# Kernel tuning notes

Hardware: AMD Instinct MI355X
Metric: run time of the kernel (lower is better)

Reference implementation:

```python
import jax, jax.numpy as jnp
import numpy as np

# dims (must match input_specs / init_kwargs)
B, N, L, D = 4, 2000, 32, 64
H, ND, K, DOUT = 4, 64, 20, 64  # num_heads, node_dim, topk, out_dim
EPS = 1e-8


def setup_inputs() -> dict:
    key = jax.random.key(0)
    ks = jax.random.split(key, 10)
    lim_emb = float(np.sqrt(6.0 / (N + ND)))  # xavier_uniform-ish for embeddings
    lim_l1 = float(np.sqrt(1.0 / H))          # torch Linear default-ish
    lim_l2 = float(np.sqrt(1.0 / (2 * H)))
    lim_w = float(np.sqrt(6.0 / (D + DOUT)))
    return {
        "x": jax.random.normal(ks[0], (B, N, L, D), dtype=jnp.float32),
        "e1": jax.random.uniform(ks[1], (H, N, ND), minval=-lim_emb, maxval=lim_emb, dtype=jnp.float32),
        "e2": jax.random.uniform(ks[2], (H, ND, N), minval=-lim_emb, maxval=lim_emb, dtype=jnp.float32),
        "temperature": jnp.ones((H,), dtype=jnp.float32),
        "ew1": jax.random.uniform(ks[3], (H, 2 * H), minval=-lim_l1, maxval=lim_l1, dtype=jnp.float32),
        "eb1": jax.random.uniform(ks[4], (2 * H,), minval=-lim_l1, maxval=lim_l1, dtype=jnp.float32),
        "ew2": jax.random.uniform(ks[5], (2 * H, 1), minval=-lim_l2, maxval=lim_l2, dtype=jnp.float32),
        "eb2": jax.random.uniform(ks[6], (1,), minval=-lim_l2, maxval=lim_l2, dtype=jnp.float32),
        "weight": jax.random.uniform(ks[7], (D, DOUT), minval=-lim_w, maxval=lim_w, dtype=jnp.float32),
        "bias": jnp.zeros((DOUT,), dtype=jnp.float32),
    }


def _graph_learner(e1, e2, temperature, ew1, eb1, ew2, eb2):
    # per-head scores: (H, N, N)
    scores = jnp.einsum("hnd,hdm->hnm", e1, e2)
    adj = jax.nn.softmax(jax.nn.relu(scores) / temperature[:, None, None], axis=-1)
    # topk sparsification along each row (dim=1 in torch == last axis here)
    _, idx = jax.lax.top_k(adj, K)  # (H, N, K)
    mask = jnp.zeros_like(adj).at[
        jnp.arange(H)[:, None, None], jnp.arange(N)[None, :, None], idx
    ].set(1.0)
    adj = adj * mask
    adj = adj / (jnp.sum(adj, axis=-1, keepdims=True) + EPS)
    # edge encoder MLP over head dim (dropout is identity in eval mode)
    feats = jnp.transpose(adj, (1, 2, 0))              # (N, N, H)
    hid = jax.nn.relu(feats @ ew1 + eb1)               # (N, N, 2H)
    ew = (hid @ ew2 + eb2)[..., 0]                     # (N, N)
    final_adj = jax.nn.sigmoid(ew) * jnp.mean(adj, axis=0)
    return final_adj, adj


def reference(x, e1, e2, temperature, ew1, eb1, ew2, eb2, weight, bias):
    final_adj, _ = _graph_learner(e1, e2, temperature, ew1, eb1, ew2, eb2)
    Bv, Nv, Lv, Dv = x.shape
    xr = jnp.transpose(x, (0, 2, 1, 3)).reshape(Bv * Lv, Nv, Dv)  # (B*L, N, D)
    support = xr @ weight                                          # (B*L, N, Dout)
    # adj.t() @ support  ->  out[b,i,:] = sum_j adj[j,i] * support[b,j,:]
    out = jnp.einsum("ji,bjd->bid", final_adj, support) + bias
    out = jnp.transpose(out.reshape(Bv, Lv, Nv, -1), (0, 2, 1, 3))  # (B, N, L, Dout)
    return out, final_adj
```

## Files before the change

kernel.cpp:

```cpp
#include <hip/hip_runtime.h>

#define NB   2000
#define HH   4
#define KK   20
#define KP   2048
#define GA   4
#define EPSF 1e-8f

typedef unsigned short ushort;
typedef unsigned long long ull;
using short8   = __attribute__((ext_vector_type(8))) short;
using floatx4  = __attribute__((ext_vector_type(4))) float;
using ushortx4 = __attribute__((ext_vector_type(4))) unsigned short;
using ushortx8 = __attribute__((ext_vector_type(8))) unsigned short;

__device__ inline ushort f2bf(float f) {
    unsigned u = __builtin_bit_cast(unsigned, f);
    u += 0x7fffu + ((u >> 16) & 1u);
    return (ushort)(u >> 16);
}

__device__ __forceinline__ void gload_lds16(const ushort* g, ushort* l) {
    __builtin_amdgcn_global_load_lds(
        (const __attribute__((address_space(1))) void*)g,
        (__attribute__((address_space(3))) void*)l, 16, 0, 0);
}

template<int CTRL>
__device__ __forceinline__ float dppmax(float x) {
    int xi = __builtin_bit_cast(int, x);
    int yi = __builtin_amdgcn_update_dpp(xi, xi, CTRL, 0xF, 0xF, false);
    return fmaxf(x, __builtin_bit_cast(float, yi));
}

__device__ __forceinline__ float wavemax63(float x) {
    x = dppmax<0x111>(x);
    x = dppmax<0x112>(x);
    x = dppmax<0x114>(x);
    x = dppmax<0x118>(x);
    x = dppmax<0x142>(x);
    x = dppmax<0x143>(x);
    return x;
}

#define COMP(v,i) ((i)==0?(v).x:(i)==1?(v).y:(i)==2?(v).z:(v).w)

__global__ __launch_bounds__(512, 4) void k_scores_topk(
    const float* __restrict__ e1, const float* __restrict__ e2,
    const float* __restrict__ temperature,
    int* __restrict__ topk_idx, float* __restrict__ topk_val)
{
    const int h  = blockIdx.y;
    const int n0 = blockIdx.x * GA;
    const int t  = threadIdx.x;
    const int w  = t >> 6, lane = t & 63;

    __shared__ float e1s[GA][64];
    __shared__ float scoresS[GA][2048];
    __shared__ float red[GA][4];
    __shared__ ull   lists[4][GA][KK + 1];
    __shared__ float selpv[GA][KK];
    __shared__ int   seli[GA][KK];
    __shared__ float ssum[GA];

    if (t < 256)
        e1s[t >> 6][t & 63] = e1[(size_t)(h * NB + n0 + (t >> 6)) * 64 + (t & 63)];
    __syncthreads();

    const float rtemp = 1.f / temperature[h];
    const float* __restrict__ e2h = e2 + (size_t)h * 64 * NB;

    {
        const int mb1 = w * 256 + lane * 4;
        const int ml1 = (mb1 < NB) ? mb1 : (NB - 4);

        float acc[GA][4];
#pragma unroll
        for (int r = 0; r < GA; r++)
#pragma unroll
            for (int c = 0; c < 4; c++) acc[r][c] = 0.f;

        for (int d4 = 0; d4 < 64; d4 += 4) {
            float4 ev0 = *(const float4*)&e1s[0][d4];
            float4 ev1 = *(const float4*)&e1s[1][d4];
            float4 ev2 = *(const float4*)&e1s[2][d4];
            float4 ev3 = *(const float4*)&e1s[3][d4];
#pragma unroll
            for (int dd = 0; dd < 4; dd++) {
                float4 a = *(const float4*)(e2h + (size_t)(d4 + dd) * NB + ml1);
                float f0 = COMP(ev0, dd), f1 = COMP(ev1, dd);
                float f2 = COMP(ev2, dd), f3 = COMP(ev3, dd);
                acc[0][0] += f0*a.x; acc[0][1] += f0*a.y; acc[0][2] += f0*a.z; acc[0][3] += f0*a.w;
                acc[1][0] += f1*a.x; acc[1][1] += f1*a.y; acc[1][2] += f1*a.z; acc[1][3] += f1*a.w;
                acc[2][0] += f2*a.x; acc[2][1] += f2*a.y; acc[2][2] += f2*a.z; acc[2][3] += f2*a.w;
                acc[3][0] += f3*a.x; acc[3][1] += f3*a.y; acc[3][2] += f3*a.z; acc[3][3] += f3*a.w;
            }
        }

#pragma unroll
        for (int r = 0; r < GA; r++) {
            float4 v; v.x = acc[r][0]; v.y = acc[r][1]; v.z = acc[r][2]; v.w = acc[r][3];
            *(float4*)&scoresS[r][mb1] = v;
        }
    }
    __syncthreads();

    if (w < 4) {
        const int  mbase = w * 512 + lane * 8;
        const bool valid = (mbase < NB);

        float acc[GA][8];
#pragma unroll
        for (int r = 0; r < GA; r++) {
            float4 lo = *(const float4*)&scoresS[r][mbase];
            float4 hi = *(const float4*)&scoresS[r][mbase + 4];
            acc[r][0] = lo.x; acc[r][1] = lo.y; acc[r][2] = lo.z; acc[r][3] = lo.w;
            acc[r][4] = hi.x; acc[r][5] = hi.y; acc[r][6] = hi.z; acc[r][7] = hi.w;
        }

#pragma unroll
        for (int r = 0; r < GA; r++) {
            float tvm = -1.f;
#pragma unroll
            for (int k = 0; k < 8; k++) {
                float v = valid ? fmaxf(acc[r][k], 0.f) * rtemp : -1.f;
                acc[r][k] = v;
                tvm = fmaxf(tvm, v);
            }
            tvm = wavemax63(tvm);
            if (lane == 63) red[r][w] = tvm;
        }

        float lm[GA]; int ak[GA];
#pragma unroll
        for (int r = 0; r < GA; r++) {
            float l = acc[r][0]; int a = 0;
#pragma unroll
            for (int k = 1; k < 8; k++)
                if (acc[r][k] > l) { l = acc[r][k]; a = k; }
            lm[r] = l; ak[r] = a;
        }

        for (int round = 0; round < KK; round++) {
            float M[GA];
#pragma unroll
            for (int r = 0; r < GA; r++) M[r] = lm[r];
#pragma unroll
            for (int r = 0; r < GA; r++) M[r] = dppmax<0x111>(M[r]);
#pragma unroll
            for (int r = 0; r < GA; r++) M[r] = dppmax<0x112>(M[r]);
#pragma unroll
            for (int r = 0; r < GA; r++) M[r] = dppmax<0x114>(M[r]);
#pragma unroll
            for (int r = 0; r < GA; r++) M[r] = dppmax<0x118>(M[r]);
#pragma unroll
            for (int r = 0; r < GA; r++) M[r] = dppmax<0x142>(M[r]);
#pragma unroll
            for (int r = 0; r < GA; r++) M[r] = dppmax<0x143>(M[r]);
#pragma unroll
            for (int r = 0; r < GA; r++)
                M[r] = __builtin_bit_cast(float,
                         __builtin_amdgcn_readlane(__builtin_bit_cast(int, M[r]), 63));
#pragma unroll
            for (int r = 0; r < GA; r++) {
                ull ball = __ballot(lm[r] == M[r]);
                int wl   = __ffsll(ball) - 1;
                if (lane == wl) {
                    int gidx = mbase + ak[r];
                    lists[w][r][round] =
                        ((ull)__float_as_uint(M[r]) << 32) | (unsigned)~gidx;
#pragma unroll
                    for (int k = 0; k < 8; k++) if (k == ak[r]) acc[r][k] = -2.f;
                    float l = acc[r][0]; int a = 0;
#pragma unroll
                    for (int k = 1; k < 8; k++)
                        if (acc[r][k] > l) { l = acc[r][k]; a = k; }
                    lm[r] = l; ak[r] = a;
                }
            }
        }
#pragma unroll
        for (int r = 0; r < GA; r++)
            if (lane == 0) lists[w][r][KK] = 0ULL;
    }
    __syncthreads();

    if (t < GA) {
        const int r = t;
        float mx = fmaxf(fmaxf(red[r][0], red[r][1]), fmaxf(red[r][2], red[r][3]));
        int p0 = 0, p1 = 0, p2 = 0, p3 = 0;
        ull h0 = lists[0][r][0], h1 = lists[1][r][0];
        ull h2 = lists[2][r][0], h3 = lists[3][r][0];
        float ss = 0.f;
        for (int q = 0; q < KK; q++) {
            ull a_ = h0 >= h1 ? h0 : h1; int wa = h0 >= h1 ? 0 : 1;
            ull b_ = h2 >= h3 ? h2 : h3; int wb = h2 >= h3 ? 2 : 3;
            ull bk = a_ >= b_ ? a_ : b_; int bw = a_ >= b_ ? wa : wb;
            float tvv = __uint_as_float((unsigned)(bk >> 32));
            float pv  = __expf(tvv - mx);
            selpv[r][q] = pv;
            seli[r][q]  = (int)~(unsigned)bk;
            ss += pv;
            if      (bw == 0) h0 = lists[0][r][++p0];
            else if (bw == 1) h1 = lists[1][r][++p1];
            else if (bw == 2) h2 = lists[2][r][++p2];
            else              h3 = lists[3][r][++p3];
        }
        ssum[r] = ss;
    }
    __syncthreads();

    if (t < GA * KK) {
        int r = t / KK, q = t % KK;
        int o = (h * NB + n0 + r) * KK + q;
        topk_idx[o] = seli[r][q];
        topk_val[o] = selpv[r][q] / (ssum[r] + EPSF);
    }
}

__global__ __launch_bounds__(256) void k_final_adj(
    const int* __restrict__ topk_idx, const float* __restrict__ topk_val,
    const float* __restrict__ ew1, const float* __restrict__ eb1,
    const float* __restrict__ ew2, const float* __restrict__ eb2,
    float* __restrict__ fadj_out, ushort* __restrict__ faT_b)
{
    const int i = blockIdx.x;
    const int t = threadIdx.x;

    __shared__ float rows[HH][NB];
    __shared__ float w1[32];
    __shared__ float b1[8];
    __shared__ float w2[8];
    __shared__ float b2v;

    for (int k = t; k < HH * NB; k += 256) ((float*)rows)[k] = 0.f;
    if (t < 32) w1[t] = ew1[t];
    if (t < 8)  { b1[t] = eb1[t]; w2[t] = ew2[t]; }
    if (t == 0) b2v = eb2[0];
    __syncthreads();

    if (t < HH * KK) {
        int h = t / KK, r = t % KK;
        int o = (h * NB + i) * KK + r;
        rows[h][topk_idx[o]] = topk_val[o];
    }
    __syncthreads();

#pragma unroll
    for (int k = 0; k < 8; k++) {
        int j = k * 256 + t;
        if (j < NB) {
            float f0 = rows[0][j], f1 = rows[1][j], f2 = rows[2][j], f3 = rows[3][j];
            float mean = (f0 + f1 + f2 + f3) * 0.25f;
            float outv = 0.f;
            if (mean > 0.f) {
                float ewv = b2v;
#pragma unroll
                for (int c = 0; c < 8; c++) {
                    float hid = f0 * w1[c] + f1 * w1[8 + c] + f2 * w1[16 + c] + f3 * w1[24 + c] + b1[c];
                    hid = fmaxf(hid, 0.f);
                    ewv += hid * w2[c];
                }
                float sig = 1.f / (1.f + expf(-ewv));
                outv = sig * mean;
                faT_b[(size_t)j * KP + i] = f2bf(outv);
            }
            fadj_out[(size_t)i * NB + j] = outv;
        }
    }
}

__global__ __launch_bounds__(256) void k_support_t(
    const float* __restrict__ x, const float* __restrict__ w,
    ushort* __restrict__ ST)
{
    const int jt = blockIdx.x;
    const int bl = blockIdx.y;
    const int b_ = bl >> 5, l = bl & 31;
    const int t  = threadIdx.x;

    __shared__ float  xs[64][65];
    __shared__ float  ws[64 * 64];
    __shared__ ushort ob[64 * 65];

    for (int k = t; k < 4096; k += 256) ws[k] = w[k];

    {
        const float* xb = x + (size_t)b_ * 4096000 + (size_t)l * 64;
#pragma unroll
        for (int p = 0; p < 4; p++) {
            int q  = p * 256 + t;
            int jl = q >> 4, f4 = q & 15;
            int jg = jt * 64 + jl;
            int jc = jg < NB ? jg : (NB - 1);
            *(float4*)&xs[jl][f4 * 4] =
                *(const float4*)(xb + (size_t)jc * 2048 + f4 * 4);
        }
    }
    __syncthreads();

    const int dq = t & 15;
    const int g  = t >> 4;
    float acc[4][4];
#pragma unroll
    for (int r = 0; r < 4; r++)
#pragma unroll
        for (int c = 0; c < 4; c++) acc[r][c] = 0.f;

    for (int dd = 0; dd < 64; dd++) {
        float4 w4 = *(const float4*)&ws[dd * 64 + dq * 4];
#pragma unroll
        for (int r = 0; r < 4; r++) {
            float xv = xs[g * 4 + r][dd];
            acc[r][0] += xv * w4.x;
            acc[r][1] += xv * w4.y;
            acc[r][2] += xv * w4.z;
            acc[r][3] += xv * w4.w;
        }
    }

#pragma unroll
    for (int r = 0; r < 4; r++) {
        int jl = g * 4 + r;
        bool jvalid = (jt * 64 + jl) < NB;
        ushort* dst = &ob[jl * 65 + dq * 4];
        dst[0] = jvalid ? f2bf(acc[r][0]) : (ushort)0;
        dst[1] = jvalid ? f2bf(acc[r][1]) : (ushort)0;
        dst[2] = jvalid ? f2bf(acc[r][2]) : (ushort)0;
        dst[3] = jvalid ? f2bf(acc[r][3]) : (ushort)0;
    }
    __syncthreads();

#pragma unroll
    for (int p = 0; p < 2; p++) {
        int q = p * 256 + t;
        int rc = q >> 3, s = q & 7;
        ushortx8 o;
#pragma unroll
        for (int k = 0; k < 8; k++) o[k] = ob[(s * 8 + k) * 65 + rc];
        *(ushortx8*)&ST[(size_t)(bl * 64 + rc) * KP + jt * 64 + s * 8] = o;
    }
}

__global__ __launch_bounds__(256) void k_gemm(
    const ushort* __restrict__ A, const ushort* __restrict__ B,
    const float* __restrict__ bias, float* __restrict__ out)
{
    __shared__ ushort As[128 * 64];
    __shared__ ushort Bs[128 * 64];

    const int t    = threadIdx.x;
    const int lane = t & 63, wave = t >> 6;
    const int wm   = wave & 1, wn = wave >> 1;

    const int lin = blockIdx.y * 16 + blockIdx.x;
    const int tl  = (lin & 7) * 128 + (lin >> 3);
    const int i0  = (tl & 15) * 128;
    const int c0  = (tl >> 4) * 128;

    const int lr = lane >> 3;
    const int dg = lane & 7;

    floatx4 acc[4][4];
#pragma unroll
    for (int r = 0; r < 4; r++)
#pragma unroll
        for (int c = 0; c < 4; c++) acc[r][c] = (floatx4)(0.f);

    for (int kb = 0; kb < 32; kb++) {
        __syncthreads();
#pragma unroll
        for (int p = 0; p < 4; p++) {
            int rowb = p * 32 + wave * 8;
            int row  = rowb + lr;
            int g    = dg ^ lr;
            const ushort* ga = &A[(size_t)(i0 + row) * KP + kb * 64 + g * 8];
            const ushort* gb = &B[(size_t)(c0 + row) * KP + kb * 64 + g * 8];
            gload_lds16(ga, &As[rowb * 64]);
            gload_lds16(gb, &Bs[rowb * 64]);
        }
        __syncthreads();

#pragma unroll
        for (int kk = 0; kk < 2; kk++) {
            short8 af[4], bf[4];
            const int gidx = kk * 4 + (lane >> 4);
            const int dsw  = gidx ^ (lane & 7);
#pragma unroll
            for (int r = 0; r < 4; r++) {
                int m = wm * 64 + r * 16 + (lane & 15);
                af[r] = *(const short8*)&As[m * 64 + dsw * 8];
            }
#pragma unroll
            for (int c = 0; c < 4; c++) {
                int m = wn * 64 + c * 16 + (lane & 15);
                bf[c] = *(const short8*)&Bs[m * 64 + dsw * 8];
            }
#pragma unroll
            for (int r = 0; r < 4; r++)
#pragma unroll
                for (int c = 0; c < 4; c++)
                    acc[r][c] = __builtin_amdgcn_mfma_f32_16x16x32_bf16(af[r], bf[c], acc[r][c], 0, 0, 0);
        }
    }

    const int mq = (lane >> 4) * 4;
    const int nn = lane & 15;
#pragma unroll
    for (int r = 0; r < 4; r++) {
#pragma unroll
        for (int c = 0; c < 4; c++) {
            int cg = c0 + wn * 64 + c * 16 + nn;
            float bv = bias[cg & 63];
            int b_ = cg >> 11, rem = cg & 2047;
            float* op = out + (size_t)b_ * 4096000 + rem;
#pragma unroll
            for (int rg = 0; rg < 4; rg++) {
                int i = i0 + wm * 64 + r * 16 + mq + rg;
                if (i < NB) op[(size_t)i * 2048] = acc[r][c][rg] + bv;
            }
        }
    }
}

extern "C" void kernel_launch(void* const* d_in, const int* in_sizes, int n_in,
                              void* d_out, int out_size, void* d_ws, size_t ws_size,
                              hipStream_t stream)
{
    const float* x           = (const float*)d_in[0];
    const float* e1          = (const float*)d_in[1];
    const float* e2          = (const float*)d_in[2];
    const float* temperature = (const float*)d_in[3];
    const float* ew1         = (const float*)d_in[4];
    const float* eb1         = (const float*)d_in[5];
    const float* ew2         = (const float*)d_in[6];
    const float* eb2         = (const float*)d_in[7];
    const float* weight      = (const float*)d_in[8];
    const float* bias        = (const float*)d_in[9];

    float* out  = (float*)d_out;
    float* fadj = out + 16384000;

    ushort* ST       = (ushort*)d_ws;
    ushort* faT_b    = ST + (size_t)8192 * KP;
    int*    topk_idx = (int*)(faT_b + (size_t)KP * KP);
    float*  topk_val = (float*)(topk_idx + 160000);

    hipMemsetAsync(faT_b, 0, (size_t)KP * KP * sizeof(ushort), stream);

    k_scores_topk<<<dim3(NB / GA, HH), 512, 0, stream>>>(e1, e2, temperature,
                                                         topk_idx, topk_val);
    k_final_adj<<<NB, 256, 0, stream>>>(topk_idx, topk_val, ew1, eb1, ew2, eb2,
                                        fadj, faT_b);
    k_support_t<<<dim3(32, 128), 256, 0, stream>>>(x, weight, ST);
    k_gemm<<<dim3(16, 64), 256, 0, stream>>>(faT_b, ST, bias, out);
}
```

Before: 372.3 us.

## Double-buffer LDS and enlarge GEMM tiles to 256x256 with 512 threads

The final adjacency GEMM moves from 128x128 tiles with 256 threads to 256x256 tiles with 512 threads, each wave computing a 128x64 sub-tile. LDS is double-buffered so the next K-slice loads asynchronously with global_load_lds while the current one is consumed, synchronized by explicit vmcnt waits and barriers. This aims to hide global load latency and raise data reuse per tile. In exchange it quadruples LDS use to 128KB per block, increases register pressure from the larger accumulator array, and shrinks the grid to 256 blocks.

Measured after the change: 361.7 us. 1.03x faster.

```diff
diff --git a/kernel.cpp b/kernel.cpp
--- a/kernel.cpp
+++ b/kernel.cpp
@@ -342,72 +342,90 @@
     }
 }
 
-__global__ __launch_bounds__(256) void k_gemm(
+__global__ __launch_bounds__(512, 2) void k_gemm(
     const ushort* __restrict__ A, const ushort* __restrict__ B,
     const float* __restrict__ bias, float* __restrict__ out)
 {
-    __shared__ ushort As[128 * 64];
-    __shared__ ushort Bs[128 * 64];
+    __shared__ ushort As[2][256 * 64];
+    __shared__ ushort Bs[2][256 * 64];
 
     const int t    = threadIdx.x;
     const int lane = t & 63, wave = t >> 6;
-    const int wm   = wave & 1, wn = wave >> 1;
-
-    const int lin = blockIdx.y * 16 + blockIdx.x;
-    const int tl  = (lin & 7) * 128 + (lin >> 3);
-    const int i0  = (tl & 15) * 128;
-    const int c0  = (tl >> 4) * 128;
+    const int wm   = wave & 1;
+    const int wn   = wave >> 1;
+
+    const int lin = blockIdx.y * 8 + blockIdx.x;
+    const int swz = (lin & 7) * 32 + (lin >> 3);
+    const int i0  = (swz & 7) * 256;
+    const int c0  = (swz >> 3) * 256;
 
     const int lr = lane >> 3;
     const int dg = lane & 7;
 
-    floatx4 acc[4][4];
-#pragma unroll
-    for (int r = 0; r < 4; r++)
+    floatx4 acc[8][4];
+#pragma unroll
+    for (int r = 0; r < 8; r++)
 #pragma unroll
         for (int c = 0; c < 4; c++) acc[r][c] = (floatx4)(0.f);
 
+#define STAGE(buf, kb)                                                         \
+    {                                                                          \
+        _Pragma("unroll")                                                      \
+        for (int p = 0; p < 4; p++) {                                          \
+            int rowb = wave * 32 + p * 8;                                      \
+            int row  = rowb + lr;                                              \
+            int g    = dg ^ lr;                                                \
+            gload_lds16(&A[(size_t)(i0 + row) * KP + (kb) * 64 + g * 8],       \
+                        &As[buf][rowb * 64]);                                  \
+            gload_lds16(&B[(size_t)(c0 + row) * KP + (kb) * 64 + g * 8],       \
+                        &Bs[buf][rowb * 64]);                                  \
+        }                                                                      \
+    }
+
+    STAGE(0, 0);
+    int cur = 0;
+
     for (int kb = 0; kb < 32; kb++) {
-        __syncthreads();
-#pragma unroll
-        for (int p = 0; p < 4; p++) {
-            int rowb = p * 32 + wave * 8;
-            int row  = rowb + lr;
-            int g    = dg ^ lr;
-            const ushort* ga = &A[(size_t)(i0 + row) * KP + kb * 64 + g * 8];
-            const ushort* gb = &B[(size_t)(c0 + row) * KP + kb * 64 + g * 8];
-            gload_lds16(ga, &As[rowb * 64]);
-            gload_lds16(gb, &Bs[rowb * 64]);
-        }
-        __syncthreads();
+        if (kb < 31) {
+            STAGE(cur ^ 1, kb + 1);
+            asm volatile("s_waitcnt vmcnt(8)" ::: "memory");
+        } else {
+            asm volatile("s_waitcnt vmcnt(0)" ::: "memory");
+        }
+        __builtin_amdgcn_s_barrier();
+        __builtin_amdgcn_sched_barrier(0);
 
 #pragma unroll
         for (int kk = 0; kk < 2; kk++) {
-            short8 af[4], bf[4];
+            short8 af[8], bf[4];
             const int gidx = kk * 4 + (lane >> 4);
             const int dsw  = gidx ^ (lane & 7);
 #pragma unroll
-            for (int r = 0; r < 4; r++) {
-                int m = wm * 64 + r * 16 + (lane & 15);
-                af[r] = *(const short8*)&As[m * 64 + dsw * 8];
+            for (int r = 0; r < 8; r++) {
+                int m = wm * 128 + r * 16 + (lane & 15);
+                af[r] = *(const short8*)&As[cur][m * 64 + dsw * 8];
             }
 #pragma unroll
             for (int c = 0; c < 4; c++) {
                 int m = wn * 64 + c * 16 + (lane & 15);
-                bf[c] = *(const short8*)&Bs[m * 64 + dsw * 8];
-            }
-#pragma unroll
-            for (int r = 0; r < 4; r++)
+                bf[c] = *(const short8*)&Bs[cur][m * 64 + dsw * 8];
+            }
+#pragma unroll
+            for (int r = 0; r < 8; r++)
 #pragma unroll
                 for (int c = 0; c < 4; c++)
                     acc[r][c] = __builtin_amdgcn_mfma_f32_16x16x32_bf16(af[r], bf[c], acc[r][c], 0, 0, 0);
         }
-    }
+
+        __builtin_amdgcn_s_barrier();
+        cur ^= 1;
+    }
+#undef STAGE
 
     const int mq = (lane >> 4) * 4;
     const int nn = lane & 15;
 #pragma unroll
-    for (int r = 0; r < 4; r++) {
+    for (int r = 0; r < 8; r++) {
 #pragma unroll
         for (int c = 0; c < 4; c++) {
             int cg = c0 + wn * 64 + c * 16 + nn;
@@ -416,7 +434,7 @@
             float* op = out + (size_t)b_ * 4096000 + rem;
 #pragma unroll
             for (int rg = 0; rg < 4; rg++) {
-                int i = i0 + wm * 64 + r * 16 + mq + rg;
+                int i = i0 + wm * 128 + r * 16 + mq + rg;
                 if (i < NB) op[(size_t)i * 2048] = acc[r][c][rg] + bv;
             }
         }
@@ -453,5 +471,5 @@
     k_final_adj<<<NB, 256, 0, stream>>>(topk_idx, topk_val, ew1, eb1, ew2, eb2,
                                         fadj, faT_b);
     k_support_t<<<dim3(32, 128), 256, 0, stream>>>(x, weight, ST);
-    k_gemm<<<dim3(16, 64), 256, 0, stream>>>(faT_b, ST, bias, out);
-}
+    k_gemm<<<dim3(8, 32), 512, 0, stream>>>(faT_b, ST, bias, out);
+}
```
